# Kernel optimization log

Measured on AMD Instinct MI355X. Metric: run time of the kernel, lower is better.

The kernel has to match this reference:

```python
import jax, jax.numpy as jnp
import numpy as np

D_MODEL = 1024
N_HEADS = 16
D_K = D_MODEL // N_HEADS


def setup_inputs() -> dict:
    key = jax.random.key(0)
    ks = jax.random.split(key, 9)
    B, S = 4, 2048
    scale = 0.02
    x = jax.random.normal(ks[0], (B, S, D_MODEL), dtype=jnp.float32)
    mask = jnp.ones((1, 1, S, S), dtype=jnp.int32)
    wq = jax.random.normal(ks[1], (D_MODEL, D_MODEL), dtype=jnp.float32) * scale
    bq = jnp.zeros((D_MODEL,), dtype=jnp.float32)
    wk = jax.random.normal(ks[2], (D_MODEL, D_MODEL), dtype=jnp.float32) * scale
    bk = jnp.zeros((D_MODEL,), dtype=jnp.float32)
    wv = jax.random.normal(ks[3], (D_MODEL, D_MODEL), dtype=jnp.float32) * scale
    bv = jnp.zeros((D_MODEL,), dtype=jnp.float32)
    wo = jax.random.normal(ks[4], (D_MODEL, D_MODEL), dtype=jnp.float32) * scale
    bo = jnp.zeros((D_MODEL,), dtype=jnp.float32)
    return {"x": x, "mask": mask, "wq": wq, "bq": bq, "wk": wk, "bk": bk,
            "wv": wv, "bv": bv, "wo": wo, "bo": bo}


def reference(x, mask, wq, bq, wk, bk, wv, bv, wo, bo):
    B, S, _ = x.shape
    # torch Linear: y = x @ W.T + b
    def proj(w, b):
        return (jnp.einsum('bsd,ed->bse', x, w) + b).reshape(B, S, N_HEADS, D_K).transpose(0, 2, 1, 3)
    q = proj(wq, bq)  # [B,H,S,Dk]
    k = proj(wk, bk)
    v = proj(wv, bv)
    scores = jnp.einsum('bhqd,bhkd->bhqk', q, k) / jnp.sqrt(jnp.float32(D_K))
    scores = jnp.where(mask == 0, jnp.float32(-jnp.inf), scores)
    attn = jax.nn.softmax(scores, axis=-1)
    out = jnp.einsum('bhqk,bhkd->bhqd', attn, v)  # [B,H,S,Dk]
    out = out.transpose(0, 2, 1, 3).reshape(B, S, D_MODEL)
    return jnp.einsum('bsd,ed->bse', out, wo) + bo
```

## Files before the change

kernel.cpp:

```cpp
#include <hip/hip_runtime.h>
#include <hip/hip_bf16.h>
#include <math.h>
#include <stdint.h>

typedef unsigned short u16;
typedef unsigned int u32;
typedef __bf16 bf16x2 __attribute__((ext_vector_type(2)));
typedef __bf16 bf16x8 __attribute__((ext_vector_type(8)));
typedef float f32x4 __attribute__((ext_vector_type(4)));

#define AS1 __attribute__((address_space(1)))
#define AS3 __attribute__((address_space(3)))

#define QSCALE 0.18033688011112042f

__device__ __forceinline__ u16 f2bf(float f) {
  union { float f; u32 i; } c; c.f = f;
  const u32 x = c.i;
  return (u16)((x + 0x7fffu + ((x >> 16) & 1u)) >> 16);
}
#if __has_builtin(__builtin_amdgcn_cvt_pk_bf16_f32)
__device__ __forceinline__ u32 pkbf(float a, float b) {
  const bf16x2 v = __builtin_amdgcn_cvt_pk_bf16_f32(a, b);
  union { bf16x2 v; u32 i; } c; c.v = v; return c.i;
}
#else
__device__ __forceinline__ u32 pkbf(float a, float b) {
  return (u32)f2bf(a) | ((u32)f2bf(b) << 16);
}
#endif
#if __has_builtin(__builtin_amdgcn_exp2f)
#define EXP2(x) __builtin_amdgcn_exp2f(x)
#else
#define EXP2(x) __expf((x) * 0.6931471805599453f)
#endif
__device__ __forceinline__ void gload_lds16(const void* g, void* lds) {
  __builtin_amdgcn_global_load_lds((const AS1 void*)g, (AS3 void*)lds, 16, 0, 0);
}

__global__ void cast_all_kernel(const float* __restrict__ x, const float* __restrict__ wq,
                                const float* __restrict__ wk, const float* __restrict__ wv,
                                const float* __restrict__ wo, u16* __restrict__ xh,
                                u16* __restrict__ wh) {
  const int i = blockIdx.x * 256 + threadIdx.x;
  const float* src; u16* dst; int off;
  if (i < 2097152) {
    src = x; dst = xh; off = i;
  } else {
    const int j = i - 2097152;
    const int w = j >> 18;
    off = j & 262143;
    src = (w == 0) ? wq : (w == 1) ? wk : (w == 2) ? wv : wo;
    dst = wh + (size_t)w * 1048576;
  }
  const float4 v = ((const float4*)src)[off];
  ushort4 o;
  o.x = f2bf(v.x); o.y = f2bf(v.y); o.z = f2bf(v.z); o.w = f2bf(v.w);
  ((ushort4*)dst)[off] = o;
}

template <int MODE, bool SCALE>
__device__ __forceinline__ void gemm_body(const u16* __restrict__ A,
                                          const u16* __restrict__ W,
                                          const float* __restrict__ bias,
                                          void* __restrict__ out) {
  __shared__ alignas(16) u16 As[128 * 32];
  __shared__ alignas(16) u16 Bs[128 * 32];
  const int tid = threadIdx.x;
  const int wave = tid >> 6, lane = tid & 63;
  const int quad = lane >> 4, l16 = lane & 15;
  const int m0 = blockIdx.y * 128, n0 = blockIdx.x * 128;
  const int wm = (wave >> 1) * 64, wn = (wave & 1) * 64;

  f32x4 vzero = {0.f, 0.f, 0.f, 0.f};
  f32x4 acc[4][4];
#pragma unroll
  for (int i = 0; i < 4; i++)
#pragma unroll
    for (int j = 0; j < 4; j++) acc[i][j] = vzero;

  for (int k0 = 0; k0 < 1024; k0 += 32) {
#pragma unroll
    for (int p = 0; p < 2; ++p) {
      const int cbase = p * 256 + wave * 64;
      const int c = cbase + lane;
      const int row = c >> 2, kc4 = c & 3;
      gload_lds16(A + (size_t)(m0 + row) * 1024 + k0 + kc4 * 8, (char*)As + cbase * 16);
      gload_lds16(W + (size_t)(n0 + row) * 1024 + k0 + kc4 * 8, (char*)Bs + cbase * 16);
    }
    __syncthreads();
    bf16x8 af[4], bw[4];
#pragma unroll
    for (int im = 0; im < 4; im++)
      af[im] = *(const bf16x8*)&As[(wm + im * 16 + l16) * 32 + quad * 8];
#pragma unroll
    for (int in_ = 0; in_ < 4; in_++)
      bw[in_] = *(const bf16x8*)&Bs[(wn + in_ * 16 + l16) * 32 + quad * 8];
#pragma unroll
    for (int im = 0; im < 4; im++)
#pragma unroll
      for (int in_ = 0; in_ < 4; in_++)
        acc[im][in_] = __builtin_amdgcn_mfma_f32_16x16x32_bf16(af[im], bw[in_], acc[im][in_], 0, 0, 0);
    __syncthreads();
  }

#pragma unroll
  for (int in_ = 0; in_ < 4; in_++) {
    const int col = n0 + wn + in_ * 16 + l16;
    const float bvf = bias[col];
#pragma unroll
    for (int im = 0; im < 4; im++) {
#pragma unroll
      for (int r = 0; r < 4; r++) {
        const int row = m0 + wm + im * 16 + quad * 4 + r;
        float v = acc[im][in_][r] + bvf;
        if (SCALE) v *= QSCALE;
        if (MODE == 0) {
          ((float*)out)[(size_t)row * 1024 + col] = v;
        } else if (MODE == 1) {
          const int b = row >> 11, s = row & 2047;
          const int h = col >> 6, dk = col & 63;
          ((u16*)out)[((((size_t)b * 16 + h) * 2048) + s) * 64 + dk] = f2bf(v);
        } else {
          const int b = row >> 11, s = row & 2047;
          const int h = col >> 6, dk = col & 63;
          ((u16*)out)[(((size_t)(b * 16 + h) * 64 + dk) * 2048) + s] = f2bf(v);
        }
      }
    }
  }
}

__global__ __launch_bounds__(256) void gemm_qkv_kernel(
    const u16* __restrict__ x, const u16* __restrict__ wq, const u16* __restrict__ wk,
    const u16* __restrict__ wv, const float* __restrict__ bq, const float* __restrict__ bk,
    const float* __restrict__ bv, u16* __restrict__ Q, u16* __restrict__ K,
    u16* __restrict__ VT) {
  if (blockIdx.z == 0)      gemm_body<1, true >(x, wq, bq, Q);
  else if (blockIdx.z == 1) gemm_body<1, false>(x, wk, bk, K);
  else                      gemm_body<2, false>(x, wv, bv, VT);
}

__global__ __launch_bounds__(256) void gemm_o_kernel(const u16* __restrict__ A,
                                                     const u16* __restrict__ wo,
                                                     const float* __restrict__ bo,
                                                     float* __restrict__ out) {
  gemm_body<0, false>(A, wo, bo, out);
}

__global__ void mask_check_kernel(const int* __restrict__ mask, int* __restrict__ flag) {
  const int i = blockIdx.x * 256 + threadIdx.x;
  const int4 v = ((const int4*)mask)[i];
  if (v.x == 0 || v.y == 0 || v.z == 0 || v.w == 0) atomicOr(flag, 1);
}

__global__ __launch_bounds__(256) void attn_kernel(const u16* __restrict__ Q,
                                                   const u16* __restrict__ K,
                                                   const u16* __restrict__ VT,
                                                   const int* __restrict__ mask,
                                                   const int* __restrict__ flag,
                                                   u16* __restrict__ O) {
  __shared__ alignas(16) u16 Ks[64 * 64];
  __shared__ alignas(16) u16 Vt[64 * 64];
  __shared__ alignas(16) u16 Ps[4 * 1024];

  const int tid = threadIdx.x;
  const int wave = tid >> 6, lane = tid & 63;
  const int quad = lane >> 4, l16 = lane & 15;
  const int qt = blockIdx.x, bh = blockIdx.y;
  const int b = bh >> 4, h = bh & 15;
  const int q0 = qt * 64;
  const u16* Qh = Q + (size_t)bh * 2048 * 64;
  const u16* Kh = K + (size_t)bh * 2048 * 64;
  const u16* Vth = VT + (size_t)bh * 64 * 2048;
  u16* Pw = Ps + wave * 1024;
  const bool masked = (*flag != 0);

  bf16x8 aq[2];
  {
    const u16* qrow = Qh + (size_t)(q0 + wave * 16 + l16) * 64 + quad * 8;
    aq[0] = *(const bf16x8*)qrow;
    aq[1] = *(const bf16x8*)(qrow + 32);
  }

  f32x4 vzero = {0.f, 0.f, 0.f, 0.f};
  f32x4 acc[4];
#pragma unroll
  for (int jd = 0; jd < 4; jd++) acc[jd] = vzero;
  float lp[4] = {0.f, 0.f, 0.f, 0.f};

  for (int kb = 0; kb < 32; ++kb) {
    const int key0 = kb * 64;
#pragma unroll
    for (int p = 0; p < 2; ++p) {
      const int cbase = p * 256 + wave * 64;
      const int c = cbase + lane;
      const int row = c >> 3, cc = c & 7;
      gload_lds16(Kh + (size_t)(key0 + row) * 64 + ((cc ^ (row & 7)) << 3),
                  (char*)Ks + cbase * 16);
      gload_lds16(Vth + (size_t)row * 2048 + key0 + ((cc ^ (row & 7)) << 3),
                  (char*)Vt + cbase * 16);
    }
    __syncthreads();

    float pe[4][4];
#pragma unroll
    for (int jn = 0; jn < 4; jn++) {
      f32x4 sc = vzero;
#pragma unroll
      for (int kc = 0; kc < 2; kc++) {
        const int r_ = jn * 16 + l16;
        const bf16x8 bk_ = *(const bf16x8*)
            &Ks[r_ * 64 + (((kc * 4 + quad) ^ (l16 & 7)) << 3)];
        sc = __builtin_amdgcn_mfma_f32_16x16x32_bf16(aq[kc], bk_, sc, 0, 0, 0);
      }
      if (masked) {
#pragma unroll
        for (int r = 0; r < 4; r++) {
          const int qg = q0 + wave * 16 + quad * 4 + r;
          const int kg = key0 + jn * 16 + l16;
          if (mask[(size_t)qg * 2048 + kg] == 0) sc[r] = -INFINITY;
        }
      }
#pragma unroll
      for (int r = 0; r < 4; r++) {
        const float p = EXP2(sc[r]);
        pe[jn][r] = p;
        lp[r] += p;
      }
    }

#pragma unroll
    for (int jn = 0; jn < 4; jn++)
#pragma unroll
      for (int r = 0; r < 4; r += 2) {
        const u32 pk = pkbf(pe[jn][r], pe[jn][r + 1]);
        const int q_a = quad * 4 + r, q_b = q_a + 1;
        Pw[q_a * 64 + (((jn * 2 + (l16 >> 3)) ^ (q_a & 7)) << 3) + (l16 & 7)] = (u16)pk;
        Pw[q_b * 64 + (((jn * 2 + (l16 >> 3)) ^ (q_b & 7)) << 3) + (l16 & 7)] = (u16)(pk >> 16);
      }

    bf16x8 ap[2];
#pragma unroll
    for (int kc = 0; kc < 2; kc++)
      ap[kc] = *(const bf16x8*)&Pw[l16 * 64 + (((kc * 4 + quad) ^ (l16 & 7)) << 3)];
#pragma unroll
    for (int jd = 0; jd < 4; jd++) {
#pragma unroll
      for (int kc = 0; kc < 2; kc++) {
        const int dk_ = jd * 16 + l16;
        const bf16x8 bv_ = *(const bf16x8*)
            &Vt[dk_ * 64 + (((kc * 4 + quad) ^ (l16 & 7)) << 3)];
        acc[jd] = __builtin_amdgcn_mfma_f32_16x16x32_bf16(ap[kc], bv_, acc[jd], 0, 0, 0);
      }
    }
    __syncthreads();
  }

  float linv[4];
#pragma unroll
  for (int r = 0; r < 4; r++) {
    float ls = lp[r];
#pragma unroll
    for (int off = 1; off < 16; off <<= 1) ls += __shfl_xor(ls, off, 16);
    linv[r] = 1.0f / ls;
  }
#pragma unroll
  for (int jd = 0; jd < 4; jd++) {
#pragma unroll
    for (int r = 0; r < 4; r++) {
      const int qg = q0 + wave * 16 + quad * 4 + r;
      const size_t token = (size_t)b * 2048 + qg;
      const int col = h * 64 + jd * 16 + l16;
      O[token * 1024 + col] = f2bf(acc[jd][r] * linv[r]);
    }
  }
}

extern "C" void kernel_launch(void* const* d_in, const int* in_sizes, int n_in,
                              void* d_out, int out_size, void* d_ws, size_t ws_size,
                              hipStream_t stream) {
  const float* x  = (const float*)d_in[0];
  const int* mask = (const int*)d_in[1];
  const float* wq = (const float*)d_in[2];
  const float* bq = (const float*)d_in[3];
  const float* wk = (const float*)d_in[4];
  const float* bk = (const float*)d_in[5];
  const float* wv = (const float*)d_in[6];
  const float* bv = (const float*)d_in[7];
  const float* wo = (const float*)d_in[8];
  const float* bo = (const float*)d_in[9];
  float* out = (float*)d_out;

  u16* xh = (u16*)d_ws;
  u16* wh = xh + 8388608;
  u16* Qw = wh + 4194304;
  u16* Kw = Qw + 8388608;
  u16* Vw = Kw + 8388608;
  int* mflag = (int*)(Vw + 8388608);
  u16* Ow = xh;

  hipMemsetAsync(mflag, 0, sizeof(int), stream);
  mask_check_kernel<<<4096, 256, 0, stream>>>(mask, mflag);
  cast_all_kernel<<<12288, 256, 0, stream>>>(x, wq, wk, wv, wo, xh, wh);

  gemm_qkv_kernel<<<dim3(8, 64, 3), 256, 0, stream>>>(
      xh, wh + 0 * 1048576, wh + 1 * 1048576, wh + 2 * 1048576,
      bq, bk, bv, Qw, Kw, Vw);
  attn_kernel<<<dim3(32, 64), 256, 0, stream>>>(Qw, Kw, Vw, mask, mflag, Ow);
  gemm_o_kernel<<<dim3(8, 64, 1), 256, 0, stream>>>(Ow, wh + 3 * 1048576, bo, out);
}
```

Measured before the change: 344.5 us.

## Process two query tiles per attention block and vectorize V-transpose stores

The attention kernel now handles 128 queries per block: each wave computes two 16-row query tiles against every K/V tile it loads into shared memory, so K/V global traffic and barriers per query are halved. The grid shrinks to 16x64 blocks, and register and LDS use per block roughly double. Separately, the V projection epilogue now packs four consecutive sequence positions into one 8-byte store instead of four scattered 2-byte stores. This may lower occupancy and leaves fewer blocks to spread across CUs.

```diff
diff --git a/kernel.cpp b/kernel.cpp
--- a/kernel.cpp
+++ b/kernel.cpp
@@ -108,23 +108,33 @@
   for (int in_ = 0; in_ < 4; in_++) {
     const int col = n0 + wn + in_ * 16 + l16;
     const float bvf = bias[col];
-#pragma unroll
-    for (int im = 0; im < 4; im++) {
-#pragma unroll
-      for (int r = 0; r < 4; r++) {
-        const int row = m0 + wm + im * 16 + quad * 4 + r;
-        float v = acc[im][in_][r] + bvf;
-        if (SCALE) v *= QSCALE;
-        if (MODE == 0) {
-          ((float*)out)[(size_t)row * 1024 + col] = v;
-        } else if (MODE == 1) {
-          const int b = row >> 11, s = row & 2047;
-          const int h = col >> 6, dk = col & 63;
-          ((u16*)out)[((((size_t)b * 16 + h) * 2048) + s) * 64 + dk] = f2bf(v);
-        } else {
-          const int b = row >> 11, s = row & 2047;
-          const int h = col >> 6, dk = col & 63;
-          ((u16*)out)[(((size_t)(b * 16 + h) * 64 + dk) * 2048) + s] = f2bf(v);
+    if (MODE == 2) {
+      const int h = col >> 6, dk = col & 63;
+#pragma unroll
+      for (int im = 0; im < 4; im++) {
+        const int row0 = m0 + wm + im * 16 + quad * 4;
+        const int b = row0 >> 11, s = row0 & 2047;
+        const u32 lo = pkbf(acc[im][in_][0] + bvf, acc[im][in_][1] + bvf);
+        const u32 hi = pkbf(acc[im][in_][2] + bvf, acc[im][in_][3] + bvf);
+        u16* base = (u16*)out + ((size_t)(b * 16 + h) * 64 + dk) * 2048 + s;
+        uint2 pkd; pkd.x = lo; pkd.y = hi;
+        *(uint2*)base = pkd;
+      }
+    } else {
+#pragma unroll
+      for (int im = 0; im < 4; im++) {
+#pragma unroll
+        for (int r = 0; r < 4; r++) {
+          const int row = m0 + wm + im * 16 + quad * 4 + r;
+          float v = acc[im][in_][r] + bvf;
+          if (SCALE) v *= QSCALE;
+          if (MODE == 0) {
+            ((float*)out)[(size_t)row * 1024 + col] = v;
+          } else {
+            const int b = row >> 11, s = row & 2047;
+            const int h = col >> 6, dk = col & 63;
+            ((u16*)out)[((((size_t)b * 16 + h) * 2048) + s) * 64 + dk] = f2bf(v);
+          }
         }
       }
     }
@@ -162,32 +172,35 @@
                                                    u16* __restrict__ O) {
   __shared__ alignas(16) u16 Ks[64 * 64];
   __shared__ alignas(16) u16 Vt[64 * 64];
-  __shared__ alignas(16) u16 Ps[4 * 1024];
+  __shared__ alignas(16) u16 Ps[4 * 2048];
 
   const int tid = threadIdx.x;
   const int wave = tid >> 6, lane = tid & 63;
   const int quad = lane >> 4, l16 = lane & 15;
-  const int qt = blockIdx.x, bh = blockIdx.y;
+  const int qt_ = blockIdx.x, bh = blockIdx.y;
   const int b = bh >> 4, h = bh & 15;
-  const int q0 = qt * 64;
+  const int q0 = qt_ * 128;
   const u16* Qh = Q + (size_t)bh * 2048 * 64;
   const u16* Kh = K + (size_t)bh * 2048 * 64;
   const u16* Vth = VT + (size_t)bh * 64 * 2048;
-  u16* Pw = Ps + wave * 1024;
+  u16* Pw = Ps + wave * 2048;
   const bool masked = (*flag != 0);
 
-  bf16x8 aq[2];
-  {
-    const u16* qrow = Qh + (size_t)(q0 + wave * 16 + l16) * 64 + quad * 8;
-    aq[0] = *(const bf16x8*)qrow;
-    aq[1] = *(const bf16x8*)(qrow + 32);
+  bf16x8 aq[2][2];
+#pragma unroll
+  for (int qt = 0; qt < 2; qt++) {
+    const u16* qrow = Qh + (size_t)(q0 + qt * 64 + wave * 16 + l16) * 64 + quad * 8;
+    aq[qt][0] = *(const bf16x8*)qrow;
+    aq[qt][1] = *(const bf16x8*)(qrow + 32);
   }
 
   f32x4 vzero = {0.f, 0.f, 0.f, 0.f};
-  f32x4 acc[4];
-#pragma unroll
-  for (int jd = 0; jd < 4; jd++) acc[jd] = vzero;
-  float lp[4] = {0.f, 0.f, 0.f, 0.f};
+  f32x4 acc[2][4];
+#pragma unroll
+  for (int qt = 0; qt < 2; qt++)
+#pragma unroll
+    for (int jd = 0; jd < 4; jd++) acc[qt][jd] = vzero;
+  float lp[2][4] = {{0.f, 0.f, 0.f, 0.f}, {0.f, 0.f, 0.f, 0.f}};
 
   for (int kb = 0; kb < 32; ++kb) {
     const int key0 = kb * 64;
@@ -203,47 +216,51 @@
     }
     __syncthreads();
 
-    float pe[4][4];
 #pragma unroll
     for (int jn = 0; jn < 4; jn++) {
-      f32x4 sc = vzero;
+      f32x4 sc0 = vzero, sc1 = vzero;
 #pragma unroll
       for (int kc = 0; kc < 2; kc++) {
         const int r_ = jn * 16 + l16;
         const bf16x8 bk_ = *(const bf16x8*)
             &Ks[r_ * 64 + (((kc * 4 + quad) ^ (l16 & 7)) << 3)];
-        sc = __builtin_amdgcn_mfma_f32_16x16x32_bf16(aq[kc], bk_, sc, 0, 0, 0);
+        sc0 = __builtin_amdgcn_mfma_f32_16x16x32_bf16(aq[0][kc], bk_, sc0, 0, 0, 0);
+        sc1 = __builtin_amdgcn_mfma_f32_16x16x32_bf16(aq[1][kc], bk_, sc1, 0, 0, 0);
       }
       if (masked) {
 #pragma unroll
         for (int r = 0; r < 4; r++) {
-          const int qg = q0 + wave * 16 + quad * 4 + r;
           const int kg = key0 + jn * 16 + l16;
-          if (mask[(size_t)qg * 2048 + kg] == 0) sc[r] = -INFINITY;
+          const int qa = q0 + wave * 16 + quad * 4 + r;
+          if (mask[(size_t)qa * 2048 + kg] == 0) sc0[r] = -INFINITY;
+          if (mask[(size_t)(qa + 64) * 2048 + kg] == 0) sc1[r] = -INFINITY;
         }
       }
+      float pe0[4], pe1[4];
 #pragma unroll
       for (int r = 0; r < 4; r++) {
-        const float p = EXP2(sc[r]);
-        pe[jn][r] = p;
-        lp[r] += p;
-      }
-    }
-
-#pragma unroll
-    for (int jn = 0; jn < 4; jn++)
+        pe0[r] = EXP2(sc0[r]); lp[0][r] += pe0[r];
+        pe1[r] = EXP2(sc1[r]); lp[1][r] += pe1[r];
+      }
 #pragma unroll
       for (int r = 0; r < 4; r += 2) {
-        const u32 pk = pkbf(pe[jn][r], pe[jn][r + 1]);
-        const int q_a = quad * 4 + r, q_b = q_a + 1;
-        Pw[q_a * 64 + (((jn * 2 + (l16 >> 3)) ^ (q_a & 7)) << 3) + (l16 & 7)] = (u16)pk;
-        Pw[q_b * 64 + (((jn * 2 + (l16 >> 3)) ^ (q_b & 7)) << 3) + (l16 & 7)] = (u16)(pk >> 16);
-      }
-
-    bf16x8 ap[2];
-#pragma unroll
-    for (int kc = 0; kc < 2; kc++)
-      ap[kc] = *(const bf16x8*)&Pw[l16 * 64 + (((kc * 4 + quad) ^ (l16 & 7)) << 3)];
+        const u32 pk0 = pkbf(pe0[r], pe0[r + 1]);
+        const u32 pk1 = pkbf(pe1[r], pe1[r + 1]);
+        const int qa = quad * 4 + r, qb = qa + 1;
+        const int sw = jn * 2 + (l16 >> 3), lo3 = l16 & 7;
+        Pw[qa * 64 + (((sw ^ (qa & 7)) << 3)) + lo3] = (u16)pk0;
+        Pw[qb * 64 + (((sw ^ (qb & 7)) << 3)) + lo3] = (u16)(pk0 >> 16);
+        Pw[(16 + qa) * 64 + (((sw ^ (qa & 7)) << 3)) + lo3] = (u16)pk1;
+        Pw[(16 + qb) * 64 + (((sw ^ (qb & 7)) << 3)) + lo3] = (u16)(pk1 >> 16);
+      }
+    }
+
+    bf16x8 ap0[2], ap1[2];
+#pragma unroll
+    for (int kc = 0; kc < 2; kc++) {
+      ap0[kc] = *(const bf16x8*)&Pw[l16 * 64 + (((kc * 4 + quad) ^ (l16 & 7)) << 3)];
+      ap1[kc] = *(const bf16x8*)&Pw[(16 + l16) * 64 + (((kc * 4 + quad) ^ (l16 & 7)) << 3)];
+    }
 #pragma unroll
     for (int jd = 0; jd < 4; jd++) {
 #pragma unroll
@@ -251,28 +268,28 @@
         const int dk_ = jd * 16 + l16;
         const bf16x8 bv_ = *(const bf16x8*)
             &Vt[dk_ * 64 + (((kc * 4 + quad) ^ (l16 & 7)) << 3)];
-        acc[jd] = __builtin_amdgcn_mfma_f32_16x16x32_bf16(ap[kc], bv_, acc[jd], 0, 0, 0);
+        acc[0][jd] = __builtin_amdgcn_mfma_f32_16x16x32_bf16(ap0[kc], bv_, acc[0][jd], 0, 0, 0);
+        acc[1][jd] = __builtin_amdgcn_mfma_f32_16x16x32_bf16(ap1[kc], bv_, acc[1][jd], 0, 0, 0);
       }
     }
     __syncthreads();
   }
 
-  float linv[4];
-#pragma unroll
-  for (int r = 0; r < 4; r++) {
-    float ls = lp[r];
-#pragma unroll
-    for (int off = 1; off < 16; off <<= 1) ls += __shfl_xor(ls, off, 16);
-    linv[r] = 1.0f / ls;
-  }
-#pragma unroll
-  for (int jd = 0; jd < 4; jd++) {
+#pragma unroll
+  for (int qt = 0; qt < 2; qt++) {
 #pragma unroll
     for (int r = 0; r < 4; r++) {
-      const int qg = q0 + wave * 16 + quad * 4 + r;
+      float ls = lp[qt][r];
+#pragma unroll
+      for (int off = 1; off < 16; off <<= 1) ls += __shfl_xor(ls, off, 16);
+      const float linv = 1.0f / ls;
+      const int qg = q0 + qt * 64 + wave * 16 + quad * 4 + r;
       const size_t token = (size_t)b * 2048 + qg;
-      const int col = h * 64 + jd * 16 + l16;
-      O[token * 1024 + col] = f2bf(acc[jd][r] * linv[r]);
+#pragma unroll
+      for (int jd = 0; jd < 4; jd++) {
+        const int col = h * 64 + jd * 16 + l16;
+        O[token * 1024 + col] = f2bf(acc[qt][jd][r] * linv);
+      }
     }
   }
 }
@@ -307,6 +324,6 @@
   gemm_qkv_kernel<<<dim3(8, 64, 3), 256, 0, stream>>>(
       xh, wh + 0 * 1048576, wh + 1 * 1048576, wh + 2 * 1048576,
       bq, bk, bv, Qw, Kw, Vw);
-  attn_kernel<<<dim3(32, 64), 256, 0, stream>>>(Qw, Kw, Vw, mask, mflag, Ow);
+  attn_kernel<<<dim3(16, 64), 256, 0, stream>>>(Qw, Kw, Vw, mask, mflag, Ow);
   gemm_o_kernel<<<dim3(8, 64, 1), 256, 0, stream>>>(Ow, wh + 3 * 1048576, bo, out);
 }
```

Result: no change. 339.9 us (-1.3%).
